# Performance work log

Measured on AMD Instinct MI355X. Metric: run time of the kernel, lower is better.

## Reference

```python
import jax, jax.numpy as jnp
import numpy as np

N_NODES = 50000
N_EDGES = 800000
D_FEAT = 64


def setup_inputs() -> dict:
    key = jax.random.key(0)
    kx, ks, kd = jax.random.split(key, 3)
    x = jax.random.normal(kx, (N_NODES, D_FEAT), dtype=jnp.float32)
    src = jax.random.randint(ks, (N_EDGES,), 0, N_NODES, dtype=jnp.int64)
    dst = jax.random.randint(kd, (N_EDGES,), 0, N_NODES, dtype=jnp.int64)
    return {"x": x, "src": src, "dst": dst}


def reference(x, src, dst):
    # SGC propagation: h[v] = sum_{(u->v) in E} x[u] / sqrt(out_deg(u) * out_deg(v))
    n = x.shape[0]
    # out-degrees: count of outgoing edges per node (matches graph.out_degrees())
    deg = jax.ops.segment_sum(jnp.ones(src.shape, x.dtype), src, num_segments=n)
    # per-edge normalization coefficient 1/sqrt(deg_u * deg_v)  [E]
    norm = 1.0 / jnp.sqrt(deg[src] * deg[dst])
    # gather-multiply-scatter-sum (u_mul_e_sum): messages flow src -> dst
    h = jax.ops.segment_sum(x[src] * norm[:, None], dst, num_segments=n)
    return h
```

## Files before the change

kernel.cpp:

```cpp
#include <hip/hip_runtime.h>

#define N_NODES 50000
#define N_EDGES 800000
#define D_FEAT 64

#define NBINS 2048
#define BSORT 100
#define SORT_CHUNK (N_EDGES / BSORT)
#define NSCAN (NBINS * BSORT)
#define SCAN_BLOCK 1024
#define SCAN_BLOCKS (NSCAN / SCAN_BLOCK)
#define AGG_CAP 4096
#define NAGG ((N_NODES + 31) / 32)

#define HCHUNKS 64
#define HCHUNK (N_EDGES / HCHUNKS)
#define HWORDS ((N_NODES + 3) / 4)

#define RS_BLOCKS ((N_NODES + 255) / 256)

__global__ __launch_bounds__(256)
void hist_count_kernel(const int* __restrict__ src, const int* __restrict__ dst,
                       unsigned int* __restrict__ hp32, unsigned int* __restrict__ gh) {
    __shared__ unsigned int lh[HWORDS];
    const int b = blockIdx.x, t = threadIdx.x;
    if (b < HCHUNKS) {
        for (int i = t; i < HWORDS; i += 256) lh[i] = 0u;
        __syncthreads();
        const int4* s4 = (const int4*)(src + b * HCHUNK);
        for (int i = t; i < HCHUNK / 4; i += 256) {
            int4 v = s4[i];
            atomicAdd(&lh[v.x >> 2], 1u << ((v.x & 3) * 8));
            atomicAdd(&lh[v.y >> 2], 1u << ((v.y & 3) * 8));
            atomicAdd(&lh[v.z >> 2], 1u << ((v.z & 3) * 8));
            atomicAdd(&lh[v.w >> 2], 1u << ((v.w & 3) * 8));
        }
        __syncthreads();
        for (int w = t; w < HWORDS; w += 256)
            hp32[(size_t)b * HWORDS + w] = lh[w];
    } else {
        const int cb = b - HCHUNKS;
        for (int i = t; i < NBINS; i += 256) lh[i] = 0;
        __syncthreads();
        const int4* d4 = (const int4*)(dst + cb * SORT_CHUNK);
        for (int i = t; i < SORT_CHUNK / 4; i += 256) {
            int4 v = d4[i];
            atomicAdd(&lh[v.x >> 5], 1u);
            atomicAdd(&lh[v.y >> 5], 1u);
            atomicAdd(&lh[v.z >> 5], 1u);
            atomicAdd(&lh[v.w >> 5], 1u);
        }
        __syncthreads();
        for (int i = t; i < NBINS; i += 256) gh[(size_t)i * BSORT + cb] = lh[i];
    }
}

__global__ __launch_bounds__(SCAN_BLOCK)
void scanred_rs_kernel(const unsigned int* __restrict__ gh, unsigned int* __restrict__ partial,
                       const unsigned char* __restrict__ hp8, float* __restrict__ rs) {
    const int b = blockIdx.x;
    if (b < SCAN_BLOCKS) {
        __shared__ unsigned int wsum[SCAN_BLOCK / 64];
        int g = b * SCAN_BLOCK + threadIdx.x;
        unsigned int v = gh[g];
        for (int off = 32; off > 0; off >>= 1) v += __shfl_down(v, off, 64);
        if ((threadIdx.x & 63) == 0) wsum[threadIdx.x >> 6] = v;
        __syncthreads();
        if (threadIdx.x < SCAN_BLOCK / 64) {
            unsigned int s = wsum[threadIdx.x];
            for (int off = SCAN_BLOCK / 128; off > 0; off >>= 1) s += __shfl_down(s, off, 64);
            if (threadIdx.x == 0) partial[b] = s;
        }
    } else {
        if (threadIdx.x < 256) {
            int v = (b - SCAN_BLOCKS) * 256 + threadIdx.x;
            if (v < N_NODES) {
                unsigned int s = 0;
                #pragma unroll
                for (int c = 0; c < HCHUNKS; ++c) s += hp8[(size_t)c * (HWORDS * 4) + v];
                rs[v] = rsqrtf((float)s);
            }
        }
    }
}

__global__ __launch_bounds__(SCAN_BLOCK)
void scan_final_kernel(unsigned int* __restrict__ data, const unsigned int* __restrict__ partial) {
    __shared__ unsigned int arr[SCAN_BLOCK];
    __shared__ unsigned int pbase[256];
    const int t = threadIdx.x;
    const int g = blockIdx.x * SCAN_BLOCK + t;
    if (t < 256) pbase[t] = (t < SCAN_BLOCKS) ? partial[t] : 0u;
    __syncthreads();
    for (int off = 1; off < 256; off <<= 1) {
        unsigned int u = (t < 256 && t >= off) ? pbase[t - off] : 0u;
        __syncthreads();
        if (t < 256 && t >= off) pbase[t] += u;
        __syncthreads();
    }
    const unsigned int base = (blockIdx.x == 0) ? 0u : pbase[blockIdx.x - 1];
    unsigned int v = data[g];
    arr[t] = v;
    __syncthreads();
    for (int off = 1; off < SCAN_BLOCK; off <<= 1) {
        unsigned int u = (t >= off) ? arr[t - off] : 0u;
        __syncthreads();
        arr[t] += u;
        __syncthreads();
    }
    data[g] = base + arr[t] - v;
}

__global__ __launch_bounds__(256)
void bucket_scatter_kernel(const int* __restrict__ src, const int* __restrict__ dst,
                           const unsigned int* __restrict__ gh, unsigned int* __restrict__ keysB) {
    __shared__ unsigned int cur[NBINS];
    const int b = blockIdx.x, t = threadIdx.x;
    for (int i = t; i < NBINS; i += 256) cur[i] = gh[(size_t)i * BSORT + b];
    __syncthreads();
    const int4* s4 = (const int4*)(src + b * SORT_CHUNK);
    const int4* d4 = (const int4*)(dst + b * SORT_CHUNK);
    for (int i = t; i < SORT_CHUNK / 4; i += 256) {
        int4 s = s4[i];
        int4 d = d4[i];
        unsigned int p0 = atomicAdd(&cur[d.x >> 5], 1u);
        keysB[p0] = ((unsigned int)d.x << 16) | (unsigned int)s.x;
        unsigned int p1 = atomicAdd(&cur[d.y >> 5], 1u);
        keysB[p1] = ((unsigned int)d.y << 16) | (unsigned int)s.y;
        unsigned int p2 = atomicAdd(&cur[d.z >> 5], 1u);
        keysB[p2] = ((unsigned int)d.z << 16) | (unsigned int)s.z;
        unsigned int p3 = atomicAdd(&cur[d.w >> 5], 1u);
        keysB[p3] = ((unsigned int)d.w << 16) | (unsigned int)s.w;
    }
}

__global__ __launch_bounds__(256)
void bucket_aggregate_kernel(const float* __restrict__ x, const unsigned int* __restrict__ gh,
                             const unsigned int* __restrict__ keysB, const float* __restrict__ rs,
                             float* __restrict__ h) {
    __shared__ unsigned int ebuf[AGG_CAP];
    __shared__ unsigned int ecnt[32];
    __shared__ unsigned int eoff[33];
    const int g = blockIdx.x;
    const int t = threadIdx.x;
    const int lane = t & 63;
    const int w = t >> 6;
    const unsigned int base = gh[(size_t)g * BSORT];
    const unsigned int end  = gh[(size_t)(g + 1) * BSORT];
    const int cnt = (int)(end - base);

    if (cnt > 0 && cnt <= AGG_CAP) {
        if (t < 32) ecnt[t] = 0;
        __syncthreads();
        for (int i = t; i < cnt; i += 256) atomicAdd(&ecnt[(keysB[base + i] >> 16) & 31], 1u);
        __syncthreads();
        if (t == 0) {
            unsigned int r = 0;
            for (int k2 = 0; k2 < 32; ++k2) { eoff[k2] = r; r += ecnt[k2]; }
            eoff[32] = r;
        }
        __syncthreads();
        if (t < 32) ecnt[t] = eoff[t];
        __syncthreads();
        for (int i = t; i < cnt; i += 256) {
            unsigned int k = keysB[base + i];
            ebuf[atomicAdd(&ecnt[(k >> 16) & 31], 1u)] = k;
        }
        __syncthreads();
        for (int nl = w; nl < 32; nl += 4) {
            int node = g * 32 + nl;
            if (node >= N_NODES) continue;
            int jb = (int)eoff[nl], je = (int)eoff[nl + 1];
            float acc = 0.0f;
            int j = jb;
            for (; j + 3 < je; j += 4) {
                unsigned int s0 = ebuf[j] & 0xFFFFu,     s1 = ebuf[j + 1] & 0xFFFFu;
                unsigned int s2 = ebuf[j + 2] & 0xFFFFu, s3 = ebuf[j + 3] & 0xFFFFu;
                float w0 = rs[s0], w1 = rs[s1], w2 = rs[s2], w3 = rs[s3];
                acc = fmaf(x[(size_t)s0 * D_FEAT + lane], w0, acc);
                acc = fmaf(x[(size_t)s1 * D_FEAT + lane], w1, acc);
                acc = fmaf(x[(size_t)s2 * D_FEAT + lane], w2, acc);
                acc = fmaf(x[(size_t)s3 * D_FEAT + lane], w3, acc);
            }
            for (; j < je; ++j) {
                unsigned int s = ebuf[j] & 0xFFFFu;
                acc = fmaf(x[(size_t)s * D_FEAT + lane], rs[s], acc);
            }
            h[(size_t)node * D_FEAT + lane] = (je > jb) ? acc * rs[node] : 0.0f;
        }
    } else {
        for (int nl = w; nl < 32; nl += 4) {
            int node = g * 32 + nl;
            if (node >= N_NODES) continue;
            float acc = 0.0f;
            int any = 0;
            for (unsigned int j = base; j < end; ++j) {
                unsigned int k = keysB[j];
                if ((int)((k >> 16) & 31) == nl) {
                    unsigned int s = k & 0xFFFFu;
                    acc = fmaf(x[(size_t)s * D_FEAT + lane], rs[s], acc);
                    any = 1;
                }
            }
            h[(size_t)node * D_FEAT + lane] = any ? acc * rs[node] : 0.0f;
        }
    }
}

__global__ void fb_degree_kernel(const int* __restrict__ src, unsigned int* __restrict__ deg,
                                 int n_edges) {
    int i = blockIdx.x * blockDim.x + threadIdx.x;
    int stride = gridDim.x * blockDim.x;
    for (; i < n_edges; i += stride) atomicAdd(&deg[src[i]], 1u);
}
__global__ void fb_scatter_kernel(const float* __restrict__ x, const int* __restrict__ src,
                                  const int* __restrict__ dst, const unsigned int* __restrict__ deg,
                                  float* __restrict__ h, int n_edges) {
    const int lane = threadIdx.x & 63;
    const int wave = (int)((blockIdx.x * blockDim.x + threadIdx.x) >> 6);
    const int nwaves = (int)((gridDim.x * blockDim.x) >> 6);
    for (int e = wave; e < n_edges; e += nwaves) {
        int s = __builtin_amdgcn_readfirstlane(src[e]);
        int d = __builtin_amdgcn_readfirstlane(dst[e]);
        float norm = rsqrtf((float)deg[s] * (float)deg[d]);
        atomicAdd(&h[d * D_FEAT + lane], x[s * D_FEAT + lane] * norm);
    }
}

extern "C" void kernel_launch(void* const* d_in, const int* in_sizes, int n_in,
                              void* d_out, int out_size, void* d_ws, size_t ws_size,
                              hipStream_t stream) {
    const float* x   = (const float*)d_in[0];
    const int*   src = (const int*)d_in[1];
    const int*   dst = (const int*)d_in[2];
    float* h = (float*)d_out;

    size_t off = 0;
    unsigned int*  keysB = (unsigned int*)((char*)d_ws + off);  off += (size_t)N_EDGES * 4;
    unsigned int*  hp32  = keysB;
    unsigned int*  gh    = (unsigned int*)((char*)d_ws + off);  off += (size_t)NSCAN * 4;
    float*         rs    = (float*)((char*)d_ws + off);         off += (size_t)N_NODES * 4;
    unsigned int*  spart = (unsigned int*)((char*)d_ws + off);  off += 256 * 4;

    if (ws_size >= off) {
        hist_count_kernel<<<dim3(HCHUNKS + BSORT), dim3(256), 0, stream>>>(src, dst, hp32, gh);
        scanred_rs_kernel<<<dim3(SCAN_BLOCKS + RS_BLOCKS), dim3(SCAN_BLOCK), 0, stream>>>(
            gh, spart, (const unsigned char*)hp32, rs);
        scan_final_kernel<<<dim3(SCAN_BLOCKS), dim3(SCAN_BLOCK), 0, stream>>>(gh, spart);
        bucket_scatter_kernel<<<dim3(BSORT), dim3(256), 0, stream>>>(src, dst, gh, keysB);
        bucket_aggregate_kernel<<<dim3(NAGG), dim3(256), 0, stream>>>(x, gh, keysB, rs, h);
    } else {
        unsigned int* deg = (unsigned int*)d_ws;
        hipMemsetAsync(deg, 0, N_NODES * sizeof(unsigned int), stream);
        hipMemsetAsync(d_out, 0, (size_t)out_size * sizeof(float), stream);
        fb_degree_kernel<<<dim3(1024), dim3(256), 0, stream>>>(src, deg, N_EDGES);
        fb_scatter_kernel<<<dim3(2048), dim3(256), 0, stream>>>(x, src, dst, deg, h, N_EDGES);
    }
}
```

Before: 65.33 us.

## Vectorize aggregation with float4 loads over 4 edges per wave and enlarge scatter blocks

The aggregation inner loop now splits each 64-lane wave into four 16-lane groups. Each group handles a different edge and loads a float4 slice of the source row, and the partial sums are combined with cross-lane shuffles before a float4 store by 16 lanes. This raises memory-level parallelism and the width of each load, in exchange for extra shuffles and tail handling. Separately, the bucket scatter kernel moves from 256 to 1024 threads per block to give its 100 blocks more parallelism. The larger blocks also add more contention on the shared-memory atomics.

```diff
diff --git a/kernel.cpp b/kernel.cpp
--- a/kernel.cpp
+++ b/kernel.cpp
@@ -111,16 +111,16 @@
     data[g] = base + arr[t] - v;
 }
 
-__global__ __launch_bounds__(256)
+__global__ __launch_bounds__(1024)
 void bucket_scatter_kernel(const int* __restrict__ src, const int* __restrict__ dst,
                            const unsigned int* __restrict__ gh, unsigned int* __restrict__ keysB) {
     __shared__ unsigned int cur[NBINS];
     const int b = blockIdx.x, t = threadIdx.x;
-    for (int i = t; i < NBINS; i += 256) cur[i] = gh[(size_t)i * BSORT + b];
+    for (int i = t; i < NBINS; i += 1024) cur[i] = gh[(size_t)i * BSORT + b];
     __syncthreads();
     const int4* s4 = (const int4*)(src + b * SORT_CHUNK);
     const int4* d4 = (const int4*)(dst + b * SORT_CHUNK);
-    for (int i = t; i < SORT_CHUNK / 4; i += 256) {
+    for (int i = t; i < SORT_CHUNK / 4; i += 1024) {
         int4 s = s4[i];
         int4 d = d4[i];
         unsigned int p0 = atomicAdd(&cur[d.x >> 5], 1u);
@@ -167,26 +167,58 @@
             ebuf[atomicAdd(&ecnt[(k >> 16) & 31], 1u)] = k;
         }
         __syncthreads();
+
+        const int grp = lane >> 4;
+        const int fl  = lane & 15;
         for (int nl = w; nl < 32; nl += 4) {
             int node = g * 32 + nl;
             if (node >= N_NODES) continue;
-            int jb = (int)eoff[nl], je = (int)eoff[nl + 1];
-            float acc = 0.0f;
-            int j = jb;
-            for (; j + 3 < je; j += 4) {
-                unsigned int s0 = ebuf[j] & 0xFFFFu,     s1 = ebuf[j + 1] & 0xFFFFu;
-                unsigned int s2 = ebuf[j + 2] & 0xFFFFu, s3 = ebuf[j + 3] & 0xFFFFu;
-                float w0 = rs[s0], w1 = rs[s1], w2 = rs[s2], w3 = rs[s3];
-                acc = fmaf(x[(size_t)s0 * D_FEAT + lane], w0, acc);
-                acc = fmaf(x[(size_t)s1 * D_FEAT + lane], w1, acc);
-                acc = fmaf(x[(size_t)s2 * D_FEAT + lane], w2, acc);
-                acc = fmaf(x[(size_t)s3 * D_FEAT + lane], w3, acc);
-            }
-            for (; j < je; ++j) {
-                unsigned int s = ebuf[j] & 0xFFFFu;
-                acc = fmaf(x[(size_t)s * D_FEAT + lane], rs[s], acc);
-            }
-            h[(size_t)node * D_FEAT + lane] = (je > jb) ? acc * rs[node] : 0.0f;
+            const int jb = (int)eoff[nl];
+            const int m  = (int)eoff[nl + 1] - jb;
+            float ax = 0.0f, ay = 0.0f, az = 0.0f, aw = 0.0f;
+            int jj = 0;
+            for (; jj + 8 <= m; jj += 8) {
+                unsigned int s0 = ebuf[jb + jj + grp] & 0xFFFFu;
+                unsigned int s1 = ebuf[jb + jj + 4 + grp] & 0xFFFFu;
+                const float4 v0 = *(const float4*)&x[(size_t)s0 * D_FEAT + fl * 4];
+                const float4 v1 = *(const float4*)&x[(size_t)s1 * D_FEAT + fl * 4];
+                float w0 = rs[s0], w1 = rs[s1];
+                ax = fmaf(v0.x, w0, ax); ay = fmaf(v0.y, w0, ay);
+                az = fmaf(v0.z, w0, az); aw = fmaf(v0.w, w0, aw);
+                ax = fmaf(v1.x, w1, ax); ay = fmaf(v1.y, w1, ay);
+                az = fmaf(v1.z, w1, az); aw = fmaf(v1.w, w1, aw);
+            }
+            if (jj < m) {
+                int idx = jj + grp;
+                unsigned int s = ebuf[jb + min(idx, m - 1)] & 0xFFFFu;
+                float wgt = (idx < m) ? rs[s] : 0.0f;
+                const float4 v = *(const float4*)&x[(size_t)s * D_FEAT + fl * 4];
+                ax = fmaf(v.x, wgt, ax); ay = fmaf(v.y, wgt, ay);
+                az = fmaf(v.z, wgt, az); aw = fmaf(v.w, wgt, aw);
+                jj += 4;
+                if (jj < m) {
+                    idx = jj + grp;
+                    unsigned int s2 = ebuf[jb + min(idx, m - 1)] & 0xFFFFu;
+                    float wgt2 = (idx < m) ? rs[s2] : 0.0f;
+                    const float4 v2 = *(const float4*)&x[(size_t)s2 * D_FEAT + fl * 4];
+                    ax = fmaf(v2.x, wgt2, ax); ay = fmaf(v2.y, wgt2, ay);
+                    az = fmaf(v2.z, wgt2, az); aw = fmaf(v2.w, wgt2, aw);
+                }
+            }
+            ax += __shfl_xor(ax, 16, 64); ay += __shfl_xor(ay, 16, 64);
+            az += __shfl_xor(az, 16, 64); aw += __shfl_xor(aw, 16, 64);
+            ax += __shfl_xor(ax, 32, 64); ay += __shfl_xor(ay, 32, 64);
+            az += __shfl_xor(az, 32, 64); aw += __shfl_xor(aw, 32, 64);
+            if (lane < 16) {
+                float4 o;
+                if (m > 0) {
+                    const float rsn = rs[node];
+                    o.x = ax * rsn; o.y = ay * rsn; o.z = az * rsn; o.w = aw * rsn;
+                } else {
+                    o.x = o.y = o.z = o.w = 0.0f;
+                }
+                *(float4*)&h[(size_t)node * D_FEAT + fl * 4] = o;
+            }
         }
     } else {
         for (int nl = w; nl < 32; nl += 4) {
@@ -247,7 +279,7 @@
         scanred_rs_kernel<<<dim3(SCAN_BLOCKS + RS_BLOCKS), dim3(SCAN_BLOCK), 0, stream>>>(
             gh, spart, (const unsigned char*)hp32, rs);
         scan_final_kernel<<<dim3(SCAN_BLOCKS), dim3(SCAN_BLOCK), 0, stream>>>(gh, spart);
-        bucket_scatter_kernel<<<dim3(BSORT), dim3(256), 0, stream>>>(src, dst, gh, keysB);
+        bucket_scatter_kernel<<<dim3(BSORT), dim3(1024), 0, stream>>>(src, dst, gh, keysB);
         bucket_aggregate_kernel<<<dim3(NAGG), dim3(256), 0, stream>>>(x, gh, keysB, rs, h);
     } else {
         unsigned int* deg = (unsigned int*)d_ws;
```

Measured after the change: 62.52 us. 4.3% less time.
